# Optimization experiments

Measured on AMD Instinct MI355X. Metric: run time of the kernel, lower is better.

The kernel has to match this reference:

```python
import jax, jax.numpy as jnp
import numpy as np

N_NODES = 80000
N_EDGES = 1280000
NODE_DIM = 32
EDGE_DIM = 16
HIDDEN = 64
N_HIDDEN_LAYERS = 3  # layer_count - 1
NUM_GRAPHS = 256


def setup_inputs() -> dict:
    key = jax.random.key(0)
    ks = jax.random.split(key, 16)
    s = 0.05
    H = jax.random.normal(ks[0], (N_NODES, NODE_DIM), dtype=jnp.float32)
    Xe = jax.random.normal(ks[1], (N_EDGES, EDGE_DIM), dtype=jnp.float32)
    id_Xe = jax.random.randint(ks[2], (2, N_EDGES), 0, N_NODES, dtype=jnp.int32).astype(jnp.int64)
    batch_idx = jnp.sort(jax.random.randint(ks[3], (N_NODES,), 0, NUM_GRAPHS, dtype=jnp.int32)).astype(jnp.int64)
    # input layer: M: (node+edge)->hidden, U: (hidden+node)->hidden
    Mw0 = jax.random.normal(ks[4], (NODE_DIM + EDGE_DIM, HIDDEN), dtype=jnp.float32) * s
    Mb0 = jnp.zeros((HIDDEN,), dtype=jnp.float32)
    Uw0 = jax.random.normal(ks[5], (HIDDEN + NODE_DIM, HIDDEN), dtype=jnp.float32) * s
    Ub0 = jnp.zeros((HIDDEN,), dtype=jnp.float32)
    # hidden layers: M: (hidden+edge)->hidden, U: (2*hidden)->hidden (stacked)
    Mw_h = jax.random.normal(ks[6], (N_HIDDEN_LAYERS, HIDDEN + EDGE_DIM, HIDDEN), dtype=jnp.float32) * s
    Mb_h = jnp.zeros((N_HIDDEN_LAYERS, HIDDEN), dtype=jnp.float32)
    Uw_h = jax.random.normal(ks[7], (N_HIDDEN_LAYERS, 2 * HIDDEN, HIDDEN), dtype=jnp.float32) * s
    Ub_h = jnp.zeros((N_HIDDEN_LAYERS, HIDDEN), dtype=jnp.float32)
    # final linear head hidden -> 1
    Ww = jax.random.normal(ks[8], (HIDDEN, 1), dtype=jnp.float32) * s
    Wb = jnp.zeros((1,), dtype=jnp.float32)
    return {"H": H, "Xe": Xe, "id_Xe": id_Xe, "batch_idx": batch_idx,
            "Mw0": Mw0, "Mb0": Mb0, "Uw0": Uw0, "Ub0": Ub0,
            "Mw_h": Mw_h, "Mb_h": Mb_h, "Uw_h": Uw_h, "Ub_h": Ub_h,
            "Ww": Ww, "Wb": Wb}


def reference(H, Xe, id_Xe, batch_idx, Mw0, Mb0, Uw0, Ub0, Mw_h, Mb_h, Uw_h, Ub_h, Ww, Wb):
    n = H.shape[0]
    src = id_Xe[0]
    dst = id_Xe[1]

    def gnn_layer(h, Mw, Mb, Uw, Ub):
        # message: gather source node features, concat edge features, MLP M
        m = jax.nn.relu(jnp.concatenate([h[src], Xe], axis=-1) @ Mw + Mb)  # [E, hidden]
        # scatter-sum to target nodes
        agg = jax.ops.segment_sum(m, dst, num_segments=n)  # [N, hidden]
        # update: concat node state with aggregated message, MLP U
        return jax.nn.relu(jnp.concatenate([h, agg], axis=-1) @ Uw + Ub)

    y = gnn_layer(H, Mw0, Mb0, Uw0, Ub0)
    for i in range(Mw_h.shape[0]):
        y = gnn_layer(y, Mw_h[i], Mb_h[i], Uw_h[i], Ub_h[i])

    pooled = jax.ops.segment_sum(y, batch_idx, num_segments=NUM_GRAPHS)  # [G, hidden]
    return pooled @ Ww + Wb  # [G, 1]
```

## Files before the change

### kernel.cpp

```cpp
#include <hip/hip_runtime.h>
#include <hip/hip_fp16.h>

#define HID 64

struct alignas(8)  H4 { __half2 a, b; };
struct alignas(16) H8 { __half2 h[4]; };

typedef _Float16 h2n __attribute__((ext_vector_type(2)));

__device__ inline float dot2f(__half2 a, __half2 b, float c) {
#if __has_builtin(__builtin_amdgcn_fdot2)
    h2n an, bn;
    __builtin_memcpy(&an, &a, 4);
    __builtin_memcpy(&bn, &b, 4);
    return __builtin_amdgcn_fdot2(an, bn, c, false);
#else
    float2 af = __half22float2(a), bf = __half22float2(b);
    return c + af.x * bf.x + af.y * bf.y;
#endif
}

__global__ __launch_bounds__(256) void deg_count(const int* __restrict__ dst,
                                                 int* __restrict__ deg, int E) {
    int e = blockIdx.x * 256 + threadIdx.x;
    if (e < E) atomicAdd(&deg[dst[e]], 1);
}

__global__ __launch_bounds__(256) void scan1(const int* __restrict__ deg,
                                             int* __restrict__ rowptr,
                                             int* __restrict__ bsums, int N) {
    __shared__ int s[256];
    const int t = threadIdx.x;
    const int base = blockIdx.x * 2048 + t * 8;
    int v[8], tot = 0;
    #pragma unroll
    for (int i = 0; i < 8; i++) {
        int x = (base + i < N) ? deg[base + i] : 0;
        v[i] = tot; tot += x;
    }
    s[t] = tot; __syncthreads();
    for (int off = 1; off < 256; off <<= 1) {
        int a = (t >= off) ? s[t - off] : 0;
        __syncthreads(); s[t] += a; __syncthreads();
    }
    const int texcl = s[t] - tot;
    #pragma unroll
    for (int i = 0; i < 8; i++)
        if (base + i < N) rowptr[base + i] = texcl + v[i];
    if (t == 255) bsums[blockIdx.x] = s[255];
}

__global__ void scan2(int* bsums, int NB) {
    if (blockIdx.x == 0 && threadIdx.x == 0) {
        int run = 0;
        for (int i = 0; i < NB; i++) { int x = bsums[i]; bsums[i] = run; run += x; }
    }
}

__global__ __launch_bounds__(256) void scan3(int* __restrict__ rowptr,
                                             const int* __restrict__ bsums,
                                             int N, int E) {
    int idx = blockIdx.x * 256 + threadIdx.x;
    if (idx < N) rowptr[idx] += bsums[idx >> 11];
    if (idx == 0) rowptr[N] = E;
}

__global__ __launch_bounds__(256) void permute_k(
    const int* __restrict__ src, const int* __restrict__ dst,
    const int* __restrict__ rowptr, int* __restrict__ cursor,
    const float* __restrict__ Xe, __half* __restrict__ Xes,
    unsigned* __restrict__ pks, int E)
{
    int e = blockIdx.x * 256 + threadIdx.x;
    if (e >= E) return;
    int d = dst[e];
    int pos = rowptr[d] + atomicAdd(&cursor[d], 1);
    pks[pos] = ((unsigned)src[e] << 5) | (unsigned)(d & 31);
    const float4* xi = (const float4*)&Xe[(size_t)e * 16];
    float4 x0 = xi[0], x1 = xi[1], x2 = xi[2], x3 = xi[3];
    H8 h0, h1;
    h0.h[0] = __float22half2_rn(make_float2(x0.x, x0.y));
    h0.h[1] = __float22half2_rn(make_float2(x0.z, x0.w));
    h0.h[2] = __float22half2_rn(make_float2(x1.x, x1.y));
    h0.h[3] = __float22half2_rn(make_float2(x1.z, x1.w));
    h1.h[0] = __float22half2_rn(make_float2(x2.x, x2.y));
    h1.h[1] = __float22half2_rn(make_float2(x2.z, x2.w));
    h1.h[2] = __float22half2_rn(make_float2(x3.x, x3.y));
    h1.h[3] = __float22half2_rn(make_float2(x3.z, x3.w));
    H8* xo = (H8*)&Xes[(size_t)pos * 16];
    xo[0] = h0; xo[1] = h1;
}

template<int K1>
__global__ __launch_bounds__(256) void pm_dual(
    const float* __restrict__ Hn,
    const float* __restrict__ Wm, const float* __restrict__ bm,
    const float* __restrict__ Wu, const float* __restrict__ bu,
    __half* __restrict__ PMh, __half* __restrict__ Th, int N)
{
    constexpr int KP = K1 + 4;
    constexpr int P4 = K1 / 4;
    __shared__ float Ws[K1 * 128];
    __shared__ float Xs[32 * KP];

    const int tid = threadIdx.x;
    for (int i = tid; i < K1 * 32; i += 256) {
        const int row = i >> 5, c4 = i & 31;
        float4 v = (c4 < 16) ? *(const float4*)&Wm[row * 64 + c4 * 4]
                             : *(const float4*)&Wu[row * 64 + (c4 - 16) * 4];
        *(float4*)&Ws[row * 128 + c4 * 4] = v;
    }
    const int nbase = blockIdx.x * 32;
    for (int i = tid; i < 32 * P4; i += 256) {
        const int nl = i / P4, part = i % P4;
        const int n = nbase + nl;
        if (n < N)
            *(float4*)&Xs[nl * KP + part * 4] =
                *(const float4*)&Hn[(size_t)n * K1 + part * 4];
    }
    __syncthreads();

    const int c0 = (tid & 31) * 4;
    const int n0 = (tid >> 5) * 4;
    const float4 bv = (c0 < 64) ? *(const float4*)&bm[c0]
                                : *(const float4*)&bu[c0 - 64];

    float4 acc[4];
    #pragma unroll
    for (int i = 0; i < 4; i++) acc[i] = bv;

    #pragma unroll 4
    for (int k = 0; k < K1; k += 4) {
        const float4 w0 = *(const float4*)&Ws[(k + 0) * 128 + c0];
        const float4 w1 = *(const float4*)&Ws[(k + 1) * 128 + c0];
        const float4 w2 = *(const float4*)&Ws[(k + 2) * 128 + c0];
        const float4 w3 = *(const float4*)&Ws[(k + 3) * 128 + c0];
        #pragma unroll
        for (int ni = 0; ni < 4; ni++) {
            const float4 xv = *(const float4*)&Xs[(n0 + ni) * KP + k];
            acc[ni].x += xv.x * w0.x + xv.y * w1.x + xv.z * w2.x + xv.w * w3.x;
            acc[ni].y += xv.x * w0.y + xv.y * w1.y + xv.z * w2.y + xv.w * w3.y;
            acc[ni].z += xv.x * w0.z + xv.y * w1.z + xv.z * w2.z + xv.w * w3.z;
            acc[ni].w += xv.x * w0.w + xv.y * w1.w + xv.z * w2.w + xv.w * w3.w;
        }
    }

    #pragma unroll
    for (int ni = 0; ni < 4; ni++) {
        const int n = nbase + n0 + ni;
        if (n < N) {
            H4 o;
            o.a = __float22half2_rn(make_float2(acc[ni].x, acc[ni].y));
            o.b = __float22half2_rn(make_float2(acc[ni].z, acc[ni].w));
            if (c0 < 64) *(H4*)&PMh[(size_t)n * 64 + c0]      = o;
            else         *(H4*)&Th [(size_t)n * 64 + c0 - 64] = o;
        }
    }
}

template<bool FUSE>
__global__ __launch_bounds__(256) void edge_fused(
    const __half*   __restrict__ PMh,
    const __half*   __restrict__ Th,
    const __half*   __restrict__ Xes,
    const unsigned* __restrict__ pks,
    const int*      __restrict__ rowptr,
    const float*    __restrict__ Mwb,
    const float*    __restrict__ Uwb,
    const float*    __restrict__ MwN,
    const float*    __restrict__ MbN,
    const float*    __restrict__ UwN,
    const float*    __restrict__ UbN,
    __half*         __restrict__ PMo,
    __half*         __restrict__ Tho,
    float*          __restrict__ Yout,
    int N)
{
    constexpr int AGP = HID + 4;
    __shared__ float aggs[32 * AGP];

    const int tid  = threadIdx.x;
    const int wv   = tid >> 6;
    const int lane = tid & 63;
    const int c0   = (lane & 15) * 4;
    const int g    = lane >> 4;

    __half2 wh[8][4];
    #pragma unroll
    for (int p = 0; p < 8; p++)
        #pragma unroll
        for (int j = 0; j < 4; j++)
            wh[p][j] = __float22half2_rn(make_float2(Mwb[(2 * p) * 64 + c0 + j],
                                                     Mwb[(2 * p + 1) * 64 + c0 + j]));

    for (int i = tid; i < 32 * AGP; i += 256) aggs[i] = 0.f;

    const int nbase  = blockIdx.x * 32;
    const int nend   = (nbase + 32 < N) ? nbase + 32 : N;
    const int estart = rowptr[nbase];
    const int eend   = rowptr[nend];
    __syncthreads();

    int pc = estart + wv * 16;
    unsigned pk_c[4], pk_n[4], pk_n2[4];
    H4 ph_c[4], ph_n[4];
    H8 xh_c[4][2], xh_n[4][2];

    if (pc < eend) {
        #pragma unroll
        for (int s = 0; s < 4; s++) {
            const int pe = pc + g * 4 + s;
            pk_c[s] = pks[pe < eend ? pe : eend - 1];
        }
        if (pc + 64 < eend) {
            #pragma unroll
            for (int s = 0; s < 4; s++) {
                const int pe = pc + 64 + g * 4 + s;
                pk_n[s] = pks[pe < eend ? pe : eend - 1];
            }
        }
        #pragma unroll
        for (int s = 0; s < 4; s++) {
            const int pe  = pc + g * 4 + s;
            const int pcl = pe < eend ? pe : eend - 1;
            ph_c[s] = *(const H4*)&PMh[(size_t)(pk_c[s] >> 5) * 64 + c0];
            const H8* xr = (const H8*)&Xes[(size_t)pcl * 16];
            xh_c[s][0] = xr[0]; xh_c[s][1] = xr[1];
        }
    }

    for (; pc < eend; pc += 64) {
        const int pn  = pc + 64;
        const int pn2 = pc + 128;

        if (pn < eend) {
            #pragma unroll
            for (int s = 0; s < 4; s++) {
                const int pe  = pn + g * 4 + s;
                const int pcl = pe < eend ? pe : eend - 1;
                ph_n[s] = *(const H4*)&PMh[(size_t)(pk_n[s] >> 5) * 64 + c0];
                const H8* xr = (const H8*)&Xes[(size_t)pcl * 16];
                xh_n[s][0] = xr[0]; xh_n[s][1] = xr[1];
            }
        }
        if (pn2 < eend) {
            #pragma unroll
            for (int s = 0; s < 4; s++) {
                const int pe = pn2 + g * 4 + s;
                pk_n2[s] = pks[pe < eend ? pe : eend - 1];
            }
        }

        int ld_prev = -1;
        float4 racc = make_float4(0.f, 0.f, 0.f, 0.f);
        #pragma unroll
        for (int s = 0; s < 4; s++) {
            const bool valid = (pc + g * 4 + s) < eend;
            const float2 pl = __half22float2(ph_c[s].a);
            const float2 pu = __half22float2(ph_c[s].b);
            float a0 = pl.x, a1 = pl.y, a2 = pu.x, a3 = pu.y;
            #pragma unroll
            for (int p = 0; p < 8; p++) {
                const __half2 xv = xh_c[s][p >> 2].h[p & 3];
                a0 = dot2f(xv, wh[p][0], a0);
                a1 = dot2f(xv, wh[p][1], a1);
                a2 = dot2f(xv, wh[p][2], a2);
                a3 = dot2f(xv, wh[p][3], a3);
            }
            float4 v;
            v.x = fmaxf(a0, 0.f); v.y = fmaxf(a1, 0.f);
            v.z = fmaxf(a2, 0.f); v.w = fmaxf(a3, 0.f);
            const int ld = valid ? (int)(pk_c[s] & 31u) : -1;
            if (ld == ld_prev) {
                racc.x += v.x; racc.y += v.y; racc.z += v.z; racc.w += v.w;
            } else {
                if (ld_prev >= 0) {
                    float* a = &aggs[ld_prev * AGP + c0];
                    atomicAdd(a + 0, racc.x); atomicAdd(a + 1, racc.y);
                    atomicAdd(a + 2, racc.z); atomicAdd(a + 3, racc.w);
                }
                racc = v; ld_prev = ld;
            }
        }
        if (ld_prev >= 0) {
            float* a = &aggs[ld_prev * AGP + c0];
            atomicAdd(a + 0, racc.x); atomicAdd(a + 1, racc.y);
            atomicAdd(a + 2, racc.z); atomicAdd(a + 3, racc.w);
        }

        #pragma unroll
        for (int s = 0; s < 4; s++) {
            pk_c[s] = pk_n[s]; pk_n[s] = pk_n2[s];
            ph_c[s] = ph_n[s];
            xh_c[s][0] = xh_n[s][0]; xh_c[s][1] = xh_n[s][1];
        }
    }

    __syncthreads();

    const int c0t = (tid & 15) * 4;
    const int r0  = tid >> 4;
    const int r1  = r0 + 16;
    const int n0g = nbase + r0, n1g = nbase + r1;
    float4 acc0 = make_float4(0.f, 0.f, 0.f, 0.f);
    float4 acc1 = make_float4(0.f, 0.f, 0.f, 0.f);
    if (n0g < N) {
        H4 th = *(const H4*)&Th[(size_t)n0g * 64 + c0t];
        float2 lo = __half22float2(th.a), hi = __half22float2(th.b);
        acc0 = make_float4(lo.x, lo.y, hi.x, hi.y);
    }
    if (n1g < N) {
        H4 th = *(const H4*)&Th[(size_t)n1g * 64 + c0t];
        float2 lo = __half22float2(th.a), hi = __half22float2(th.b);
        acc1 = make_float4(lo.x, lo.y, hi.x, hi.y);
    }
    #pragma unroll 4
    for (int k = 0; k < 64; k += 4) {
        const float4 w0 = *(const float4*)&Uwb[(k + 0) * 64 + c0t];
        const float4 w1 = *(const float4*)&Uwb[(k + 1) * 64 + c0t];
        const float4 w2 = *(const float4*)&Uwb[(k + 2) * 64 + c0t];
        const float4 w3 = *(const float4*)&Uwb[(k + 3) * 64 + c0t];
        const float4 x0 = *(const float4*)&aggs[r0 * AGP + k];
        const float4 x1 = *(const float4*)&aggs[r1 * AGP + k];
        acc0.x += x0.x * w0.x + x0.y * w1.x + x0.z * w2.x + x0.w * w3.x;
        acc0.y += x0.x * w0.y + x0.y * w1.y + x0.z * w2.y + x0.w * w3.y;
        acc0.z += x0.x * w0.z + x0.y * w1.z + x0.z * w2.z + x0.w * w3.z;
        acc0.w += x0.x * w0.w + x0.y * w1.w + x0.z * w2.w + x0.w * w3.w;
        acc1.x += x1.x * w0.x + x1.y * w1.x + x1.z * w2.x + x1.w * w3.x;
        acc1.y += x1.x * w0.y + x1.y * w1.y + x1.z * w2.y + x1.w * w3.y;
        acc1.z += x1.x * w0.z + x1.y * w1.z + x1.z * w2.z + x1.w * w3.z;
        acc1.w += x1.x * w0.w + x1.y * w1.w + x1.z * w2.w + x1.w * w3.w;
    }
    float4 y0, y1;
    y0.x = fmaxf(acc0.x, 0.f); y0.y = fmaxf(acc0.y, 0.f);
    y0.z = fmaxf(acc0.z, 0.f); y0.w = fmaxf(acc0.w, 0.f);
    y1.x = fmaxf(acc1.x, 0.f); y1.y = fmaxf(acc1.y, 0.f);
    y1.z = fmaxf(acc1.z, 0.f); y1.w = fmaxf(acc1.w, 0.f);

    if (!FUSE) {
        if (n0g < N) *(float4*)&Yout[(size_t)n0g * HID + c0t] = y0;
        if (n1g < N) *(float4*)&Yout[(size_t)n1g * HID + c0t] = y1;
    } else {
        __syncthreads();
        *(float4*)&aggs[r0 * AGP + c0t] = y0;
        *(float4*)&aggs[r1 * AGP + c0t] = y1;
        __syncthreads();

        const int c2  = (tid & 31) * 4;
        const int nn0 = (tid >> 5) * 4;
        const bool isM = (c2 < 64);
        const float* Wn = isM ? MwN : UwN;
        const float* bn = isM ? MbN : UbN;
        const int cc = isM ? c2 : c2 - 64;
        const float4 bv = *(const float4*)&bn[cc];
        float4 p0 = bv, p1 = bv, p2 = bv, p3 = bv;
        #pragma unroll 4
        for (int k = 0; k < 64; k += 4) {
            const float4 w0 = *(const float4*)&Wn[(k + 0) * 64 + cc];
            const float4 w1 = *(const float4*)&Wn[(k + 1) * 64 + cc];
            const float4 w2 = *(const float4*)&Wn[(k + 2) * 64 + cc];
            const float4 w3 = *(const float4*)&Wn[(k + 3) * 64 + cc];
            const float4 x0 = *(const float4*)&aggs[(nn0 + 0) * AGP + k];
            const float4 x1 = *(const float4*)&aggs[(nn0 + 1) * AGP + k];
            const float4 x2 = *(const float4*)&aggs[(nn0 + 2) * AGP + k];
            const float4 x3 = *(const float4*)&aggs[(nn0 + 3) * AGP + k];
            p0.x += x0.x * w0.x + x0.y * w1.x + x0.z * w2.x + x0.w * w3.x;
            p0.y += x0.x * w0.y + x0.y * w1.y + x0.z * w2.y + x0.w * w3.y;
            p0.z += x0.x * w0.z + x0.y * w1.z + x0.z * w2.z + x0.w * w3.z;
            p0.w += x0.x * w0.w + x0.y * w1.w + x0.z * w2.w + x0.w * w3.w;
            p1.x += x1.x * w0.x + x1.y * w1.x + x1.z * w2.x + x1.w * w3.x;
            p1.y += x1.x * w0.y + x1.y * w1.y + x1.z * w2.y + x1.w * w3.y;
            p1.z += x1.x * w0.z + x1.y * w1.z + x1.z * w2.z + x1.w * w3.z;
            p1.w += x1.x * w0.w + x1.y * w1.w + x1.z * w2.w + x1.w * w3.w;
            p2.x += x2.x * w0.x + x2.y * w1.x + x2.z * w2.x + x2.w * w3.x;
            p2.y += x2.x * w0.y + x2.y * w1.y + x2.z * w2.y + x2.w * w3.y;
            p2.z += x2.x * w0.z + x2.y * w1.z + x2.z * w2.z + x2.w * w3.z;
            p2.w += x2.x * w0.w + x2.y * w1.w + x2.z * w2.w + x2.w * w3.w;
            p3.x += x3.x * w0.x + x3.y * w1.x + x3.z * w2.x + x3.w * w3.x;
            p3.y += x3.x * w0.y + x3.y * w1.y + x3.z * w2.y + x3.w * w3.y;
            p3.z += x3.x * w0.z + x3.y * w1.z + x3.z * w2.z + x3.w * w3.z;
            p3.w += x3.x * w0.w + x3.y * w1.w + x3.z * w2.w + x3.w * w3.w;
        }
        float4 pr[4] = {p0, p1, p2, p3};
        #pragma unroll
        for (int ni = 0; ni < 4; ni++) {
            const int n = nbase + nn0 + ni;
            if (n < N) {
                H4 o;
                o.a = __float22half2_rn(make_float2(pr[ni].x, pr[ni].y));
                o.b = __float22half2_rn(make_float2(pr[ni].z, pr[ni].w));
                if (isM) *(H4*)&PMo[(size_t)n * 64 + cc] = o;
                else     *(H4*)&Tho[(size_t)n * 64 + cc] = o;
            }
        }
    }
}

__global__ __launch_bounds__(256) void pool_head(
    const float* __restrict__ Y, const int* __restrict__ bidx,
    const float* __restrict__ Ww, const float* __restrict__ Wb,
    float* __restrict__ out, int N)
{
    const int g = blockIdx.x;
    int a = 0, b = N;
    while (a < b) { int m = (a + b) >> 1; if (bidx[m] < g) a = m + 1; else b = m; }
    const int lo = a;
    b = N;
    while (a < b) { int m = (a + b) >> 1; if (bidx[m] < g + 1) a = m + 1; else b = m; }
    const int hi = a;

    const int tid = threadIdx.x;
    const int c4 = tid & 15, nl = tid >> 4;
    float4 s = make_float4(0.f, 0.f, 0.f, 0.f);
    for (int n = lo + nl; n < hi; n += 16) {
        const float4 v = *(const float4*)&Y[(size_t)n * HID + c4 * 4];
        s.x += v.x; s.y += v.y; s.z += v.z; s.w += v.w;
    }
    __shared__ float red[16 * 68];
    *(float4*)&red[nl * 68 + c4 * 4] = s;
    __syncthreads();
    if (tid < 64) {
        float t = 0.f;
        #pragma unroll
        for (int r = 0; r < 16; r++) t += red[r * 68 + tid];
        t *= Ww[tid];
        #pragma unroll
        for (int off = 32; off; off >>= 1) t += __shfl_down(t, off);
        if (tid == 0) out[g] = t + Wb[0];
    }
}

extern "C" void kernel_launch(void* const* d_in, const int* in_sizes, int n_in,
                              void* d_out, int out_size, void* d_ws, size_t ws_size,
                              hipStream_t stream) {
    const float* H    = (const float*)d_in[0];
    const float* Xe   = (const float*)d_in[1];
    const int*   ids  = (const int*)d_in[2];
    const int*   bidx = (const int*)d_in[3];
    const float* Mw0  = (const float*)d_in[4];
    const float* Mb0  = (const float*)d_in[5];
    const float* Uw0  = (const float*)d_in[6];
    const float* Ub0  = (const float*)d_in[7];
    const float* MwH  = (const float*)d_in[8];
    const float* MbH  = (const float*)d_in[9];
    const float* UwH  = (const float*)d_in[10];
    const float* UbH  = (const float*)d_in[11];
    const float* Ww   = (const float*)d_in[12];
    const float* Wb   = (const float*)d_in[13];
    float* out = (float*)d_out;

    const int N = in_sizes[0] / 32;
    const int E = in_sizes[1] / 16;
    const int* src = ids;
    const int* dst = ids + E;

    __half* PMa  = (__half*)d_ws;
    __half* Tha  = PMa + (size_t)N * HID;
    __half* PMb  = Tha + (size_t)N * HID;
    __half* Thb  = PMb + (size_t)N * HID;
    float*  yfin = (float*)d_ws;
    __half* Xes  = Thb + (size_t)N * HID;
    unsigned* pks = (unsigned*)(Xes + (size_t)E * 16);
    int* rowptr  = (int*)(pks + E);
    int* deg     = rowptr + (N + 1);
    int* bsums   = deg + N;

    const int NB = (N + 2047) / 2048;
    const int eblocks = (E + 255) / 256;
    const int ntile   = (N + 31) / 32;

    hipMemsetAsync(deg, 0, (size_t)N * sizeof(int), stream);
    deg_count<<<eblocks, 256, 0, stream>>>(dst, deg, E);
    scan1<<<NB, 256, 0, stream>>>(deg, rowptr, bsums, N);
    scan2<<<1, 64, 0, stream>>>(bsums, NB);
    scan3<<<(N + 255) / 256, 256, 0, stream>>>(rowptr, bsums, N, E);
    hipMemsetAsync(deg, 0, (size_t)N * sizeof(int), stream);
    permute_k<<<eblocks, 256, 0, stream>>>(src, dst, rowptr, deg,
                                           Xe, Xes, pks, E);

    const float* MwH0 = MwH;                 const float* UwH0 = UwH;
    const float* MwH1 = MwH + 80 * HID;      const float* UwH1 = UwH + 128 * HID;
    const float* MwH2 = MwH + 2 * 80 * HID;  const float* UwH2 = UwH + 2 * 128 * HID;

    pm_dual<32><<<ntile, 256, 0, stream>>>(H, Mw0, Mb0, Uw0, Ub0, PMa, Tha, N);
    edge_fused<true><<<ntile, 256, 0, stream>>>(
        PMa, Tha, Xes, pks, rowptr,
        Mw0 + 32 * HID, Uw0 + 32 * HID,
        MwH0, MbH, UwH0, UbH,
        PMb, Thb, nullptr, N);

    edge_fused<true><<<ntile, 256, 0, stream>>>(
        PMb, Thb, Xes, pks, rowptr,
        MwH0 + 64 * HID, UwH0 + 64 * HID,
        MwH1, MbH + HID, UwH1, UbH + HID,
        PMa, Tha, nullptr, N);

    edge_fused<true><<<ntile, 256, 0, stream>>>(
        PMa, Tha, Xes, pks, rowptr,
        MwH1 + 64 * HID, UwH1 + 64 * HID,
        MwH2, MbH + 2 * HID, UwH2, UbH + 2 * HID,
        PMb, Thb, nullptr, N);

    edge_fused<false><<<ntile, 256, 0, stream>>>(
        PMb, Thb, Xes, pks, rowptr,
        MwH2 + 64 * HID, UwH2 + 64 * HID,
        nullptr, nullptr, nullptr, nullptr,
        nullptr, nullptr, yfin, N);

    pool_head<<<256, 256, 0, stream>>>(yfin, bidx, Ww, Wb, out, N);
}
```

Baseline: 914.4 us.

## Stage edge features through LDS and cut registers to raise edge-kernel occupancy

The edge loop now loads edge features cooperatively, one 8-byte chunk per lane, into a double-buffered per-wave LDS slot instead of holding two H8 register sets per edge. Destination indices are packed into a single register, and the fused next-layer projection computes two nodes per pass instead of four. Launch bounds now request 8 blocks per CU. The aim is to lower VGPR pressure so more waves are resident to hide gather latency, at the cost of extra LDS traffic, LDS capacity per block, and possible spills under the tighter bound.

```diff
diff --git a/kernel.cpp b/kernel.cpp
--- a/kernel.cpp
+++ b/kernel.cpp
@@ -159,7 +159,7 @@
 }
 
 template<bool FUSE>
-__global__ __launch_bounds__(256) void edge_fused(
+__global__ __launch_bounds__(256, 8) void edge_fused(
     const __half*   __restrict__ PMh,
     const __half*   __restrict__ Th,
     const __half*   __restrict__ Xes,
@@ -176,14 +176,18 @@
     float*          __restrict__ Yout,
     int N)
 {
-    constexpr int AGP = HID + 4;
+    constexpr int AGP  = HID + 4;
+    constexpr int SLOT = 48;
     __shared__ float aggs[32 * AGP];
+    __shared__ char  xsh[4][2][16 * SLOT];
 
     const int tid  = threadIdx.x;
     const int wv   = tid >> 6;
     const int lane = tid & 63;
     const int c0   = (lane & 15) * 4;
     const int g    = lane >> 4;
+    const int laneE = lane >> 2;
+    const int laneP = (lane & 3) * 8;
 
     __half2 wh[8][4];
     #pragma unroll
@@ -201,100 +205,121 @@
     const int eend   = rowptr[nend];
     __syncthreads();
 
-    int pc = estart + wv * 16;
-    unsigned pk_c[4], pk_n[4], pk_n2[4];
-    H4 ph_c[4], ph_n[4];
-    H8 xh_c[4][2], xh_n[4][2];
-
-    if (pc < eend) {
-        #pragma unroll
-        for (int s = 0; s < 4; s++) {
-            const int pe = pc + g * 4 + s;
-            pk_c[s] = pks[pe < eend ? pe : eend - 1];
-        }
-        if (pc + 64 < eend) {
+    const int pc0 = estart + wv * 16;
+
+    unsigned pk0[4], pk1[4];
+    H4       phA[4], phB[4];
+    unsigned ldpA = 0, ldpB = 0;
+    uint2    xt;
+
+#define GATH(PKB, PHB, LDPB, PCN) do {                                        \
+    unsigned l_ = 0;                                                          \
+    _Pragma("unroll")                                                         \
+    for (int s = 0; s < 4; s++) {                                             \
+        const unsigned pk_ = PKB[s];                                          \
+        PHB[s] = *(const H4*)&PMh[(size_t)(pk_ >> 5) * 64 + c0];              \
+        l_ |= (pk_ & 31u) << (8 * s);                                         \
+    }                                                                         \
+    LDPB = l_;                                                                \
+    _Pragma("unroll")                                                         \
+    for (int s = 0; s < 4; s++) {                                             \
+        const int pe_ = (PCN) + g * 4 + s;                                    \
+        PKB[s] = pks[pe_ < eend ? pe_ : eend - 1];                            \
+    }                                                                         \
+} while (0)
+
+#define LOADX(CB) do {                                                        \
+    const int pe_  = (CB) + laneE;                                            \
+    const int pcl_ = pe_ < eend ? pe_ : eend - 1;                             \
+    xt = *(const uint2*)((const char*)Xes + (size_t)pcl_ * 32 + laneP);       \
+} while (0)
+
+#define WRITEX(BUF)                                                           \
+    *(uint2*)&xsh[wv][BUF][laneE * SLOT + laneP] = xt
+
+#define COMPUTE(BUF, PH, LDP, PCC) do {                                       \
+    int ld_prev = -1;                                                         \
+    float4 racc = make_float4(0.f, 0.f, 0.f, 0.f);                            \
+    _Pragma("unroll")                                                         \
+    for (int s = 0; s < 4; s++) {                                             \
+        const int e_ = g * 4 + s;                                             \
+        const H8 x0 = *(const H8*)&xsh[wv][BUF][e_ * SLOT];                   \
+        const H8 x1 = *(const H8*)&xsh[wv][BUF][e_ * SLOT + 16];              \
+        const float2 pl = __half22float2(PH[s].a);                            \
+        const float2 pu = __half22float2(PH[s].b);                            \
+        float a0 = pl.x, a1 = pl.y, a2 = pu.x, a3 = pu.y;                     \
+        _Pragma("unroll")                                                     \
+        for (int p = 0; p < 4; p++) {                                         \
+            const __half2 xv = x0.h[p];                                       \
+            a0 = dot2f(xv, wh[p][0], a0); a1 = dot2f(xv, wh[p][1], a1);       \
+            a2 = dot2f(xv, wh[p][2], a2); a3 = dot2f(xv, wh[p][3], a3);       \
+        }                                                                     \
+        _Pragma("unroll")                                                     \
+        for (int p = 0; p < 4; p++) {                                         \
+            const __half2 xv = x1.h[p];                                       \
+            a0 = dot2f(xv, wh[p+4][0], a0); a1 = dot2f(xv, wh[p+4][1], a1);   \
+            a2 = dot2f(xv, wh[p+4][2], a2); a3 = dot2f(xv, wh[p+4][3], a3);   \
+        }                                                                     \
+        float4 v;                                                             \
+        v.x = fmaxf(a0, 0.f); v.y = fmaxf(a1, 0.f);                           \
+        v.z = fmaxf(a2, 0.f); v.w = fmaxf(a3, 0.f);                           \
+        const int ld = ((PCC) + e_ < eend)                                    \
+                     ? (int)((LDP >> (8 * s)) & 31u) : -1;                    \
+        if (ld == ld_prev) {                                                  \
+            racc.x += v.x; racc.y += v.y; racc.z += v.z; racc.w += v.w;       \
+        } else {                                                              \
+            if (ld_prev >= 0) {                                               \
+                float* a_ = &aggs[ld_prev * AGP + c0];                        \
+                atomicAdd(a_ + 0, racc.x); atomicAdd(a_ + 1, racc.y);         \
+                atomicAdd(a_ + 2, racc.z); atomicAdd(a_ + 3, racc.w);         \
+            }                                                                 \
+            racc = v; ld_prev = ld;                                           \
+        }                                                                     \
+    }                                                                         \
+    if (ld_prev >= 0) {                                                       \
+        float* a_ = &aggs[ld_prev * AGP + c0];                                \
+        atomicAdd(a_ + 0, racc.x); atomicAdd(a_ + 1, racc.y);                 \
+        atomicAdd(a_ + 2, racc.z); atomicAdd(a_ + 3, racc.w);                 \
+    }                                                                         \
+} while (0)
+
+    if (pc0 < eend) {
+        {
+            unsigned l_ = 0;
             #pragma unroll
             for (int s = 0; s < 4; s++) {
-                const int pe = pc + 64 + g * 4 + s;
-                pk_n[s] = pks[pe < eend ? pe : eend - 1];
+                const int pe = pc0 + g * 4 + s;
+                const unsigned pkc = pks[pe < eend ? pe : eend - 1];
+                phA[s] = *(const H4*)&PMh[(size_t)(pkc >> 5) * 64 + c0];
+                l_ |= (pkc & 31u) << (8 * s);
             }
-        }
-        #pragma unroll
-        for (int s = 0; s < 4; s++) {
-            const int pe  = pc + g * 4 + s;
-            const int pcl = pe < eend ? pe : eend - 1;
-            ph_c[s] = *(const H4*)&PMh[(size_t)(pk_c[s] >> 5) * 64 + c0];
-            const H8* xr = (const H8*)&Xes[(size_t)pcl * 16];
-            xh_c[s][0] = xr[0]; xh_c[s][1] = xr[1];
-        }
-    }
-
-    for (; pc < eend; pc += 64) {
-        const int pn  = pc + 64;
-        const int pn2 = pc + 128;
-
-        if (pn < eend) {
+            ldpA = l_;
             #pragma unroll
             for (int s = 0; s < 4; s++) {
-                const int pe  = pn + g * 4 + s;
-                const int pcl = pe < eend ? pe : eend - 1;
-                ph_n[s] = *(const H4*)&PMh[(size_t)(pk_n[s] >> 5) * 64 + c0];
-                const H8* xr = (const H8*)&Xes[(size_t)pcl * 16];
-                xh_n[s][0] = xr[0]; xh_n[s][1] = xr[1];
+                int pe = pc0 + 64 + g * 4 + s;
+                pk0[s] = pks[pe < eend ? pe : eend - 1];
+                pe = pc0 + 128 + g * 4 + s;
+                pk1[s] = pks[pe < eend ? pe : eend - 1];
             }
+            LOADX(pc0);
+            WRITEX(0);
         }
-        if (pn2 < eend) {
-            #pragma unroll
-            for (int s = 0; s < 4; s++) {
-                const int pe = pn2 + g * 4 + s;
-                pk_n2[s] = pks[pe < eend ? pe : eend - 1];
-            }
+
+        int pc = pc0;
+        while (true) {
+            { LOADX(pc + 64); GATH(pk0, phB, ldpB, pc + 192);
+              COMPUTE(0, phA, ldpA, pc); WRITEX(1); }
+            pc += 64; if (pc >= eend) break;
+            { LOADX(pc + 64); GATH(pk1, phA, ldpA, pc + 192);
+              COMPUTE(1, phB, ldpB, pc); WRITEX(0); }
+            pc += 64; if (pc >= eend) break;
         }
-
-        int ld_prev = -1;
-        float4 racc = make_float4(0.f, 0.f, 0.f, 0.f);
-        #pragma unroll
-        for (int s = 0; s < 4; s++) {
-            const bool valid = (pc + g * 4 + s) < eend;
-            const float2 pl = __half22float2(ph_c[s].a);
-            const float2 pu = __half22float2(ph_c[s].b);
-            float a0 = pl.x, a1 = pl.y, a2 = pu.x, a3 = pu.y;
-            #pragma unroll
-            for (int p = 0; p < 8; p++) {
-                const __half2 xv = xh_c[s][p >> 2].h[p & 3];
-                a0 = dot2f(xv, wh[p][0], a0);
-                a1 = dot2f(xv, wh[p][1], a1);
-                a2 = dot2f(xv, wh[p][2], a2);
-                a3 = dot2f(xv, wh[p][3], a3);
-            }
-            float4 v;
-            v.x = fmaxf(a0, 0.f); v.y = fmaxf(a1, 0.f);
-            v.z = fmaxf(a2, 0.f); v.w = fmaxf(a3, 0.f);
-            const int ld = valid ? (int)(pk_c[s] & 31u) : -1;
-            if (ld == ld_prev) {
-                racc.x += v.x; racc.y += v.y; racc.z += v.z; racc.w += v.w;
-            } else {
-                if (ld_prev >= 0) {
-                    float* a = &aggs[ld_prev * AGP + c0];
-                    atomicAdd(a + 0, racc.x); atomicAdd(a + 1, racc.y);
-                    atomicAdd(a + 2, racc.z); atomicAdd(a + 3, racc.w);
-                }
-                racc = v; ld_prev = ld;
-            }
-        }
-        if (ld_prev >= 0) {
-            float* a = &aggs[ld_prev * AGP + c0];
-            atomicAdd(a + 0, racc.x); atomicAdd(a + 1, racc.y);
-            atomicAdd(a + 2, racc.z); atomicAdd(a + 3, racc.w);
-        }
-
-        #pragma unroll
-        for (int s = 0; s < 4; s++) {
-            pk_c[s] = pk_n[s]; pk_n[s] = pk_n2[s];
-            ph_c[s] = ph_n[s];
-            xh_c[s][0] = xh_n[s][0]; xh_c[s][1] = xh_n[s][1];
-        }
-    }
+    }
+
+#undef GATH
+#undef LOADX
+#undef WRITEX
+#undef COMPUTE
 
     __syncthreads();
 
@@ -353,44 +378,41 @@
         const float* bn = isM ? MbN : UbN;
         const int cc = isM ? c2 : c2 - 64;
         const float4 bv = *(const float4*)&bn[cc];
-        float4 p0 = bv, p1 = bv, p2 = bv, p3 = bv;
-        #pragma unroll 4
-        for (int k = 0; k < 64; k += 4) {
-            const float4 w0 = *(const float4*)&Wn[(k + 0) * 64 + cc];
-            const float4 w1 = *(const float4*)&Wn[(k + 1) * 64 + cc];
-            const float4 w2 = *(const float4*)&Wn[(k + 2) * 64 + cc];
-            const float4 w3 = *(const float4*)&Wn[(k + 3) * 64 + cc];
-            const float4 x0 = *(const float4*)&aggs[(nn0 + 0) * AGP + k];
-            const float4 x1 = *(const float4*)&aggs[(nn0 + 1) * AGP + k];
-            const float4 x2 = *(const float4*)&aggs[(nn0 + 2) * AGP + k];
-            const float4 x3 = *(const float4*)&aggs[(nn0 + 3) * AGP + k];
-            p0.x += x0.x * w0.x + x0.y * w1.x + x0.z * w2.x + x0.w * w3.x;
-            p0.y += x0.x * w0.y + x0.y * w1.y + x0.z * w2.y + x0.w * w3.y;
-            p0.z += x0.x * w0.z + x0.y * w1.z + x0.z * w2.z + x0.w * w3.z;
-            p0.w += x0.x * w0.w + x0.y * w1.w + x0.z * w2.w + x0.w * w3.w;
-            p1.x += x1.x * w0.x + x1.y * w1.x + x1.z * w2.x + x1.w * w3.x;
-            p1.y += x1.x * w0.y + x1.y * w1.y + x1.z * w2.y + x1.w * w3.y;
-            p1.z += x1.x * w0.z + x1.y * w1.z + x1.z * w2.z + x1.w * w3.z;
-            p1.w += x1.x * w0.w + x1.y * w1.w + x1.z * w2.w + x1.w * w3.w;
-            p2.x += x2.x * w0.x + x2.y * w1.x + x2.z * w2.x + x2.w * w3.x;
-            p2.y += x2.x * w0.y + x2.y * w1.y + x2.z * w2.y + x2.w * w3.y;
-            p2.z += x2.x * w0.z + x2.y * w1.z + x2.z * w2.z + x2.w * w3.z;
-            p2.w += x2.x * w0.w + x2.y * w1.w + x2.z * w2.w + x2.w * w3.w;
-            p3.x += x3.x * w0.x + x3.y * w1.x + x3.z * w2.x + x3.w * w3.x;
-            p3.y += x3.x * w0.y + x3.y * w1.y + x3.z * w2.y + x3.w * w3.y;
-            p3.z += x3.x * w0.z + x3.y * w1.z + x3.z * w2.z + x3.w * w3.z;
-            p3.w += x3.x * w0.w + x3.y * w1.w + x3.z * w2.w + x3.w * w3.w;
-        }
-        float4 pr[4] = {p0, p1, p2, p3};
-        #pragma unroll
-        for (int ni = 0; ni < 4; ni++) {
-            const int n = nbase + nn0 + ni;
-            if (n < N) {
+
+        #pragma unroll 1
+        for (int h = 0; h < 2; h++) {
+            const int na = nn0 + 2 * h, nb = na + 1;
+            float4 p0 = bv, p1 = bv;
+            #pragma unroll 4
+            for (int k = 0; k < 64; k += 4) {
+                const float4 w0 = *(const float4*)&Wn[(k + 0) * 64 + cc];
+                const float4 w1 = *(const float4*)&Wn[(k + 1) * 64 + cc];
+                const float4 w2 = *(const float4*)&Wn[(k + 2) * 64 + cc];
+                const float4 w3 = *(const float4*)&Wn[(k + 3) * 64 + cc];
+                const float4 x0 = *(const float4*)&aggs[na * AGP + k];
+                const float4 x1 = *(const float4*)&aggs[nb * AGP + k];
+                p0.x += x0.x * w0.x + x0.y * w1.x + x0.z * w2.x + x0.w * w3.x;
+                p0.y += x0.x * w0.y + x0.y * w1.y + x0.z * w2.y + x0.w * w3.y;
+                p0.z += x0.x * w0.z + x0.y * w1.z + x0.z * w2.z + x0.w * w3.z;
+                p0.w += x0.x * w0.w + x0.y * w1.w + x0.z * w2.w + x0.w * w3.w;
+                p1.x += x1.x * w0.x + x1.y * w1.x + x1.z * w2.x + x1.w * w3.x;
+                p1.y += x1.x * w0.y + x1.y * w1.y + x1.z * w2.y + x1.w * w3.y;
+                p1.z += x1.x * w0.z + x1.y * w1.z + x1.z * w2.z + x1.w * w3.z;
+                p1.w += x1.x * w0.w + x1.y * w1.w + x1.z * w2.w + x1.w * w3.w;
+            }
+            if (nbase + na < N) {
                 H4 o;
-                o.a = __float22half2_rn(make_float2(pr[ni].x, pr[ni].y));
-                o.b = __float22half2_rn(make_float2(pr[ni].z, pr[ni].w));
-                if (isM) *(H4*)&PMo[(size_t)n * 64 + cc] = o;
-                else     *(H4*)&Tho[(size_t)n * 64 + cc] = o;
+                o.a = __float22half2_rn(make_float2(p0.x, p0.y));
+                o.b = __float22half2_rn(make_float2(p0.z, p0.w));
+                if (isM) *(H4*)&PMo[(size_t)(nbase + na) * 64 + cc] = o;
+                else     *(H4*)&Tho[(size_t)(nbase + na) * 64 + cc] = o;
+            }
+            if (nbase + nb < N) {
+                H4 o;
+                o.a = __float22half2_rn(make_float2(p1.x, p1.y));
+                o.b = __float22half2_rn(make_float2(p1.z, p1.w));
+                if (isM) *(H4*)&PMo[(size_t)(nbase + nb) * 64 + cc] = o;
+                else     *(H4*)&Tho[(size_t)(nbase + nb) * 64 + cc] = o;
             }
         }
     }
```

Result: slower. 1.259 ms (+37.7%).
